# Performance work log

Measured on AMD Instinct MI355X. Metric: run time of the kernel, lower is better.

Reference implementation:

```python
import jax, jax.numpy as jnp
import numpy as np

CLIP_MIN = -3.5
CLIP_MAX = 3.5
ALPHA = 0.25


def setup_inputs() -> dict:
    key = jax.random.key(0)
    x = jax.random.normal(key, (64, 2048, 256), dtype=jnp.float32)
    return {"x": x}


def reference(x):
    # clamp, then exponential moving average along time (dim 1)
    xc = jnp.clip(x, CLIP_MIN, CLIP_MAX)          # [B, T, F]
    x0 = xc[:, 0]                                  # [B, F] -> smoothed[0] = x[0]

    def step(carry, xt):
        s = ALPHA * xt + (1.0 - ALPHA) * carry
        return s, s

    # scan over time: inputs [T-1, B, F]
    _, rest = jax.lax.scan(step, x0, jnp.moveaxis(xc[:, 1:], 1, 0))
    smoothed = jnp.concatenate([x0[:, None], jnp.moveaxis(rest, 0, 1)], axis=1)
    return smoothed
```

## Files before the change

### kernel.cpp

```cpp
#include <hip/hip_runtime.h>


constexpr int B = 64;
constexpr int T = 2048;
constexpr int C = 256;
constexpr int L = 32;
constexpr int W = 24;
constexpr int NCHUNK = T / L;
constexpr int LANES = C / 2;
constexpr int ROWF2 = C / 2;

#define EMA_ALPHA 0.25f
#define EMA_BETA  0.75f

__device__ __forceinline__ float clipf(float v) {
    return fminf(fmaxf(v, -3.5f), 3.5f);
}

__device__ __forceinline__ float2 clip2(float2 v) {
    return make_float2(clipf(v.x), clipf(v.y));
}

__device__ __forceinline__ void nt_store2(float2* p, float2 v) {
    union { float2 f2; unsigned long long u; } u;
    u.f2 = v;
    __builtin_nontemporal_store(u.u, (unsigned long long*)p);
}

__global__ __launch_bounds__(256, 8) void ema_kernel(
    const float* __restrict__ x, float* __restrict__ out)
{
    const int job  = blockIdx.x * 2 + (threadIdx.x >> 7);
    const int lane = threadIdx.x & (LANES - 1);
    const int b    = job >> 6;
    const int k    = job & (NCHUNK - 1);
    const int t0   = k * L;

    const float2* __restrict__ xin = (const float2*)x;
    float2* __restrict__ o         = (float2*)out;

    int idx;
    float2 s;

    if (k == 0) {
        idx = (b * T) * ROWF2 + lane;
        s = clip2(xin[idx]);
    } else {
        idx = (b * T + (t0 - W)) * ROWF2 + lane;
        s = clip2(xin[idx]);
#pragma unroll 8
        for (int i = 0; i < W; ++i) {
            idx += ROWF2;
            float2 v = clip2(xin[idx]);
            s.x = fmaf(EMA_ALPHA, v.x, EMA_BETA * s.x);
            s.y = fmaf(EMA_ALPHA, v.y, EMA_BETA * s.y);
        }
    }

    nt_store2(&o[idx], s);
#pragma unroll 8
    for (int i = 1; i < L; ++i) {
        idx += ROWF2;
        float2 v = clip2(xin[idx]);
        s.x = fmaf(EMA_ALPHA, v.x, EMA_BETA * s.x);
        s.y = fmaf(EMA_ALPHA, v.y, EMA_BETA * s.y);
        nt_store2(&o[idx], s);
    }
}

extern "C" void kernel_launch(void* const* d_in, const int* in_sizes, int n_in,
                              void* d_out, int out_size, void* d_ws, size_t ws_size,
                              hipStream_t stream) {
    const float* x = (const float*)d_in[0];
    float* out = (float*)d_out;
    const int n_jobs = B * NCHUNK;
    ema_kernel<<<dim3(n_jobs / 2), dim3(256), 0, stream>>>(x, out);
}
```

Measured before the change: 236.9 us.

## Use float4 lanes with explicit 8-row register prefetch pipeline in EMA kernel

Each thread now handles four channels with 128-bit loads and nontemporal stores, so a 64-lane wave covers a full row and a block holds four chunk jobs. The time loop is fully unrolled, with an 8-deep software prefetch of future rows held in registers to keep more loads in flight per thread. This aims to raise memory-level parallelism and cut instruction count on a bandwidth-bound scan. The cost is higher register pressure, reflected in the occupancy hint dropping from 8 to 4, and a larger unrolled code body.

```diff
diff --git a/kernel.cpp b/kernel.cpp
--- a/kernel.cpp
+++ b/kernel.cpp
@@ -7,64 +7,91 @@
 constexpr int L = 32;
 constexpr int W = 24;
 constexpr int NCHUNK = T / L;
-constexpr int LANES = C / 2;
-constexpr int ROWF2 = C / 2;
+constexpr int ROWF4 = C / 4;
+constexpr int PF = 8;
 
-#define EMA_ALPHA 0.25f
-#define EMA_BETA  0.75f
+#define CLIP_LO -3.5f
+#define CLIP_HI  3.5f
+#define EMA_A 0.25f
+#define EMA_B 0.75f
+
+typedef float f4 __attribute__((ext_vector_type(4)));
 
 __device__ __forceinline__ float clipf(float v) {
-    return fminf(fmaxf(v, -3.5f), 3.5f);
+    return fminf(fmaxf(v, CLIP_LO), CLIP_HI);
 }
 
-__device__ __forceinline__ float2 clip2(float2 v) {
-    return make_float2(clipf(v.x), clipf(v.y));
+__device__ __forceinline__ f4 clip4(f4 v) {
+    f4 r;
+    r.x = clipf(v.x);
+    r.y = clipf(v.y);
+    r.z = clipf(v.z);
+    r.w = clipf(v.w);
+    return r;
 }
 
-__device__ __forceinline__ void nt_store2(float2* p, float2 v) {
-    union { float2 f2; unsigned long long u; } u;
-    u.f2 = v;
-    __builtin_nontemporal_store(u.u, (unsigned long long*)p);
+__device__ __forceinline__ f4 ema4(f4 s, f4 v) {
+    f4 r;
+    r.x = fmaf(EMA_A, v.x, EMA_B * s.x);
+    r.y = fmaf(EMA_A, v.y, EMA_B * s.y);
+    r.z = fmaf(EMA_A, v.z, EMA_B * s.z);
+    r.w = fmaf(EMA_A, v.w, EMA_B * s.w);
+    return r;
 }
 
-__global__ __launch_bounds__(256, 8) void ema_kernel(
+#define SLOT(j)                                                              \
+    if (r + j < N) {                                                         \
+        f4 v = clip4(p##j);                                                  \
+        s = (r + j == 0) ? v : ema4(s, v);                                   \
+        if (r + j >= SKIP)                                                   \
+            __builtin_nontemporal_store(s, op + (r + j) * ROWF4);            \
+        if (r + j + PF < N)                                                  \
+            p##j = xp[(r + j + PF) * ROWF4];                                 \
+    }
+
+template <int N, int SKIP>
+__device__ __forceinline__ void run_rows(const f4* __restrict__ xp,
+                                         f4* __restrict__ op) {
+    f4 p0 = xp[0 * ROWF4];
+    f4 p1 = xp[1 * ROWF4];
+    f4 p2 = xp[2 * ROWF4];
+    f4 p3 = xp[3 * ROWF4];
+    f4 p4 = xp[4 * ROWF4];
+    f4 p5 = xp[5 * ROWF4];
+    f4 p6 = xp[6 * ROWF4];
+    f4 p7 = xp[7 * ROWF4];
+    f4 s = {};
+#pragma unroll
+    for (int g = 0; g < (N + PF - 1) / PF; ++g) {
+        const int r = g * PF;
+        SLOT(0)
+        SLOT(1)
+        SLOT(2)
+        SLOT(3)
+        SLOT(4)
+        SLOT(5)
+        SLOT(6)
+        SLOT(7)
+    }
+}
+
+__global__ __launch_bounds__(256, 4) void ema_kernel(
     const float* __restrict__ x, float* __restrict__ out)
 {
-    const int job  = blockIdx.x * 2 + (threadIdx.x >> 7);
-    const int lane = threadIdx.x & (LANES - 1);
+    const int job  = blockIdx.x * 4 + (threadIdx.x >> 6);
+    const int lane = threadIdx.x & 63;
     const int b    = job >> 6;
     const int k    = job & (NCHUNK - 1);
     const int t0   = k * L;
+    const int tb   = (k == 0) ? 0 : (t0 - W);
 
-    const float2* __restrict__ xin = (const float2*)x;
-    float2* __restrict__ o         = (float2*)out;
-
-    int idx;
-    float2 s;
+    const f4* __restrict__ xp = (const f4*)x + ((size_t)b * T + tb) * ROWF4 + lane;
+    f4* __restrict__ op       = (f4*)out     + ((size_t)b * T + tb) * ROWF4 + lane;
 
     if (k == 0) {
-        idx = (b * T) * ROWF2 + lane;
-        s = clip2(xin[idx]);
+        run_rows<L, 0>(xp, op);
     } else {
-        idx = (b * T + (t0 - W)) * ROWF2 + lane;
-        s = clip2(xin[idx]);
-#pragma unroll 8
-        for (int i = 0; i < W; ++i) {
-            idx += ROWF2;
-            float2 v = clip2(xin[idx]);
-            s.x = fmaf(EMA_ALPHA, v.x, EMA_BETA * s.x);
-            s.y = fmaf(EMA_ALPHA, v.y, EMA_BETA * s.y);
-        }
-    }
-
-    nt_store2(&o[idx], s);
-#pragma unroll 8
-    for (int i = 1; i < L; ++i) {
-        idx += ROWF2;
-        float2 v = clip2(xin[idx]);
-        s.x = fmaf(EMA_ALPHA, v.x, EMA_BETA * s.x);
-        s.y = fmaf(EMA_ALPHA, v.y, EMA_BETA * s.y);
-        nt_store2(&o[idx], s);
+        run_rows<W + L, W>(xp, op);
     }
 }
 
@@ -74,5 +101,5 @@
     const float* x = (const float*)d_in[0];
     float* out = (float*)d_out;
     const int n_jobs = B * NCHUNK;
-    ema_kernel<<<dim3(n_jobs / 2), dim3(256), 0, stream>>>(x, out);
+    ema_kernel<<<dim3(n_jobs / 4), dim3(256), 0, stream>>>(x, out);
 }
```

Result: no change. 233.3 us (-1.5%).
